# Kernel tuning notes

Hardware: AMD Instinct MI355X
Metric: run time of the kernel (lower is better)

Reference implementation:

```python
import jax, jax.numpy as jnp
import numpy as np

N = 8192
IN_F = 256
OUT_F = 128
ALPHA = 0.2
NEG = -9000000000000000.0

def setup_inputs() -> dict:
    key = jax.random.key(0)
    k1, k2, k3, k4 = jax.random.split(key, 4)
    h = jax.random.normal(k1, (N, IN_F), dtype=jnp.float32)
    adj = jax.random.randint(k2, (N, N), 0, 2, dtype=jnp.int32)
    # xavier-uniform-like params
    limW = float(np.sqrt(6.0 / (IN_F + OUT_F)))
    W = jax.random.uniform(k3, (IN_F, OUT_F), minval=-limW, maxval=limW, dtype=jnp.float32)
    lima = float(np.sqrt(6.0 / (2 * OUT_F + 1)))
    a = jax.random.uniform(k4, (2 * OUT_F, 1), minval=-lima, maxval=lima, dtype=jnp.float32)
    return {"h": h, "adj": adj, "W": W, "a": a}

def reference(h, adj, W, a):
    Wh = h @ W  # [N, F]
    # e_ij = LeakyReLU(a1.Wh_i + a2.Wh_j) -- avoids [N,N,2F] intermediate
    a1 = a[:OUT_F, 0]  # [F]
    a2 = a[OUT_F:, 0]  # [F]
    f1 = Wh @ a1  # [N]
    f2 = Wh @ a2  # [N]
    e = jax.nn.leaky_relu(f1[:, None] + f2[None, :], negative_slope=ALPHA)  # [N,N]
    att = jnp.where(adj > 0, e, jnp.float32(NEG))
    att = jax.nn.softmax(att, axis=1)
    h_prime = att @ Wh  # [N, F]
    return h_prime
```

## Files before the change

### kernel.cpp

```cpp
#include <hip/hip_runtime.h>
#include <hip/hip_bf16.h>

#define N    8192
#define INF  256
#define OUTF 128
#define ALPHA 0.2f
#define JS   8
#define NTS  (N / JS / 32)

typedef __attribute__((ext_vector_type(8))) short bf16x8;
typedef __attribute__((ext_vector_type(4))) float f32x4;

__device__ __forceinline__ unsigned short f2bf(float x) {
    union { float f; unsigned u; } v; v.f = x;
    unsigned r = v.u + 0x7fff + ((v.u >> 16) & 1);
    return (unsigned short)(r >> 16);
}

__device__ __forceinline__ void gll16(const void* g, void* l) {
    __builtin_amdgcn_global_load_lds(
        (const __attribute__((address_space(1))) unsigned*)g,
        (__attribute__((address_space(3))) unsigned*)l, 16, 0, 0);
}

__global__ __launch_bounds__(256) void k01_prep(
        const int* __restrict__ adj, unsigned* __restrict__ bits,
        const float* __restrict__ h, const float* __restrict__ W,
        const float* __restrict__ a,
        unsigned short* __restrict__ WhTb, float* __restrict__ f1, float* __restrict__ f2) {
    __shared__ float hs[8][INF];
    const int t = threadIdx.x;

    if (blockIdx.x >= 1024) {
        const size_t g = (size_t)(blockIdx.x - 1024) * 256 + t;
        const int4* p = (const int4*)adj + g * 8;
        unsigned b = 0;
        #pragma unroll
        for (int u = 0; u < 8; ++u) {
            int4 v = p[u];
            b |= (v.x > 0 ? 1u : 0u) << (u * 4 + 0);
            b |= (v.y > 0 ? 1u : 0u) << (u * 4 + 1);
            b |= (v.z > 0 ? 1u : 0u) << (u * 4 + 2);
            b |= (v.w > 0 ? 1u : 0u) << (u * 4 + 3);
        }
        bits[g] = b;
        return;
    }

    const int i0 = blockIdx.x * 8;
    #pragma unroll
    for (int u = 0; u < 2; ++u) {
        int idx = u * 256 + t;
        int r   = idx >> 6;
        int kq  = idx & 63;
        *(float4*)&hs[r][kq * 4] = *(const float4*)(h + (size_t)(i0 + r) * INF + kq * 4);
    }
    __syncthreads();

    const int rg = t >> 5;
    const int ct = t & 31;
    float acc[4] = {0.f, 0.f, 0.f, 0.f};

    #pragma unroll 8
    for (int k = 0; k < INF; ++k) {
        float4 wv = *(const float4*)(W + (size_t)k * OUTF + ct * 4);
        float  hx = hs[rg][k];
        acc[0] += hx * wv.x; acc[1] += hx * wv.y;
        acc[2] += hx * wv.z; acc[3] += hx * wv.w;
    }

    const int r0 = i0 + rg;
    const int jb = r0 >> 5;
    const int jo = r0 & 31;
    #pragma unroll
    for (int cc = 0; cc < 4; ++cc)
        WhTb[(size_t)jb * 4096 + (ct * 4 + cc) * 32 + jo] = f2bf(acc[cc]);

    const float4 a1v = *(const float4*)(a + ct * 4);
    const float4 a2v = *(const float4*)(a + OUTF + ct * 4);
    float p1 = acc[0]*a1v.x + acc[1]*a1v.y + acc[2]*a1v.z + acc[3]*a1v.w;
    float p2 = acc[0]*a2v.x + acc[1]*a2v.y + acc[2]*a2v.z + acc[3]*a2v.w;
    #pragma unroll
    for (int off = 16; off > 0; off >>= 1) {
        p1 += __shfl_down(p1, off, 32);
        p2 += __shfl_down(p2, off, 32);
    }
    if (ct == 0) { f1[r0] = p1; f2[r0] = p2; }
}

__device__ __forceinline__ float pbit(float f1r, float fv, unsigned byte_,
                                      int u, float& dsum) {
    float s = f1r + fv;
    float e = fmaxf(s, ALPHA * s);
    float p = (byte_ & (1u << u)) ? __expf(e) : 0.f;
    dsum += p;
    return p;
}

#define K2SUB(WORD, PH, JT)                                                  \
    {                                                                        \
        if ((JT) + 1 < NTS) {                                                \
            const char* ws_ = (const char*)WhTb + (size_t)(tile0 + (JT) + 1) * 8192; \
            char* bd_ = (char*)&bsm[(PH) ^ 1][0];                            \
            gll16(ws_ + t * 16,        bd_ + wv * 1024 + 0);                 \
            gll16(ws_ + 4096 + t * 16, bd_ + 4096 + wv * 1024 + 0);          \
        }                                                                    \
        float4 F0_ = *(const float4*)&f2s[(JT) * 32 + quad * 8];             \
        float4 F1_ = *(const float4*)&f2s[(JT) * 32 + quad * 8 + 4];         \
        unsigned byte_ = ((WORD) >> (quad << 3)) & 0xffu;                    \
        float p0_ = pbit(f1r, F0_.x, byte_, 0, dsum);                        \
        float p1_ = pbit(f1r, F0_.y, byte_, 1, dsum);                        \
        float p2_ = pbit(f1r, F0_.z, byte_, 2, dsum);                        \
        float p3_ = pbit(f1r, F0_.w, byte_, 3, dsum);                        \
        float p4_ = pbit(f1r, F1_.x, byte_, 4, dsum);                        \
        float p5_ = pbit(f1r, F1_.y, byte_, 5, dsum);                        \
        float p6_ = pbit(f1r, F1_.z, byte_, 6, dsum);                        \
        float p7_ = pbit(f1r, F1_.w, byte_, 7, dsum);                        \
        union { __hip_bfloat162 hh[4]; bf16x8 v; } pk_;                      \
        pk_.hh[0] = __float22bfloat162_rn(make_float2(p0_, p1_));            \
        pk_.hh[1] = __float22bfloat162_rn(make_float2(p2_, p3_));            \
        pk_.hh[2] = __float22bfloat162_rn(make_float2(p4_, p5_));            \
        pk_.hh[3] = __float22bfloat162_rn(make_float2(p6_, p7_));            \
        bf16x8 afrag = pk_.v;                                                \
        const char* bb_ = (const char*)&bsm[PH][0] + laneb2;                 \
        bf16x8 b0_ = *(const bf16x8*)(bb_);                                  \
        bf16x8 b1_ = *(const bf16x8*)(bb_ + 1024);                           \
        bf16x8 b2_ = *(const bf16x8*)(bb_ + 2048);                           \
        bf16x8 b3_ = *(const bf16x8*)(bb_ + 3072);                           \
        bf16x8 b4_ = *(const bf16x8*)(bb_ + 4096);                           \
        bf16x8 b5_ = *(const bf16x8*)(bb_ + 5120);                           \
        bf16x8 b6_ = *(const bf16x8*)(bb_ + 6144);                           \
        bf16x8 b7_ = *(const bf16x8*)(bb_ + 7168);                           \
        acc0 = __builtin_amdgcn_mfma_f32_16x16x32_bf16(afrag, b0_, acc0, 0, 0, 0); \
        acc1 = __builtin_amdgcn_mfma_f32_16x16x32_bf16(afrag, b1_, acc1, 0, 0, 0); \
        acc2 = __builtin_amdgcn_mfma_f32_16x16x32_bf16(afrag, b2_, acc2, 0, 0, 0); \
        acc3 = __builtin_amdgcn_mfma_f32_16x16x32_bf16(afrag, b3_, acc3, 0, 0, 0); \
        acc4 = __builtin_amdgcn_mfma_f32_16x16x32_bf16(afrag, b4_, acc4, 0, 0, 0); \
        acc5 = __builtin_amdgcn_mfma_f32_16x16x32_bf16(afrag, b5_, acc5, 0, 0, 0); \
        acc6 = __builtin_amdgcn_mfma_f32_16x16x32_bf16(afrag, b6_, acc6, 0, 0, 0); \
        acc7 = __builtin_amdgcn_mfma_f32_16x16x32_bf16(afrag, b7_, acc7, 0, 0, 0); \
        __syncthreads();                                                     \
    }

__global__ __launch_bounds__(256, 4) void k2_attn(
        const unsigned* __restrict__ bits, const unsigned short* __restrict__ WhTb,
        const float* __restrict__ f1, const float* __restrict__ f2,
        float* __restrict__ num, float* __restrict__ den) {
    __shared__ unsigned short bsm[2][4096];
    __shared__ float f2s[1024];

    const int t    = threadIdx.x;
    const int wv   = t >> 6;
    const int ln   = t & 63;
    const int m16  = ln & 15;
    const int quad = ln >> 4;
    const int i0   = blockIdx.x * 64;
    const int s    = blockIdx.y;
    const int row  = i0 + wv * 16 + m16;
    const int tile0 = s * NTS;
    const int j0    = s * (N / JS);
    const int laneb2 = (m16 * 32 + quad * 8) * 2;

    *(float4*)&f2s[t * 4] = *(const float4*)(f2 + j0 + t * 4);
    {
        const char* ws0 = (const char*)WhTb + (size_t)tile0 * 8192;
        char* bd = (char*)&bsm[0][0];
        gll16(ws0 + t * 16,        bd + wv * 1024);
        gll16(ws0 + 4096 + t * 16, bd + 4096 + wv * 1024);
    }

    const float f1r = f1[row];
    const uint4* brow = (const uint4*)(bits + (size_t)row * 256 + tile0);

    f32x4 acc0 = {0.f,0.f,0.f,0.f}, acc1 = {0.f,0.f,0.f,0.f};
    f32x4 acc2 = {0.f,0.f,0.f,0.f}, acc3 = {0.f,0.f,0.f,0.f};
    f32x4 acc4 = {0.f,0.f,0.f,0.f}, acc5 = {0.f,0.f,0.f,0.f};
    f32x4 acc6 = {0.f,0.f,0.f,0.f}, acc7 = {0.f,0.f,0.f,0.f};
    float dsum = 0.f;

    uint4 bwc = brow[0];
    __syncthreads();

    for (int g = 0; g < NTS / 4; ++g) {
        uint4 bwn = brow[(g + 1 < NTS / 4) ? g + 1 : g];
        const int jtb = g * 4;
        K2SUB(bwc.x, 0, jtb + 0)
        K2SUB(bwc.y, 1, jtb + 1)
        K2SUB(bwc.z, 0, jtb + 2)
        K2SUB(bwc.w, 1, jtb + 3)
        bwc = bwn;
    }

    dsum += __shfl_xor(dsum, 16);
    dsum += __shfl_xor(dsum, 32);
    if (quad == 0) den[(size_t)s * N + row] = dsum;

    float* np = num + (size_t)s * N * OUTF;
    #pragma unroll
    for (int r = 0; r < 4; ++r) {
        const size_t orow = (size_t)(i0 + wv * 16 + quad * 4 + r) * OUTF;
        np[orow + 0 * 16 + m16] = acc0[r];
        np[orow + 1 * 16 + m16] = acc1[r];
        np[orow + 2 * 16 + m16] = acc2[r];
        np[orow + 3 * 16 + m16] = acc3[r];
        np[orow + 4 * 16 + m16] = acc4[r];
        np[orow + 5 * 16 + m16] = acc5[r];
        np[orow + 6 * 16 + m16] = acc6[r];
        np[orow + 7 * 16 + m16] = acc7[r];
    }
}

__global__ __launch_bounds__(256) void k3_combine(
        const float* __restrict__ num, const float* __restrict__ den,
        float* __restrict__ out) {
    const int idx = blockIdx.x * 256 + threadIdx.x;
    const int row = idx >> 5;
    const int c4  = (idx & 31) * 4;
    float4 ns = {0.f,0.f,0.f,0.f};
    float  ds = 0.f;
    #pragma unroll
    for (int s = 0; s < JS; ++s) {
        float4 nv = *(const float4*)(num + ((size_t)s * N + row) * OUTF + c4);
        ns.x += nv.x; ns.y += nv.y; ns.z += nv.z; ns.w += nv.w;
        ds += den[(size_t)s * N + row];
    }
    const float inv = 1.0f / ds;
    float4 o = {ns.x * inv, ns.y * inv, ns.z * inv, ns.w * inv};
    *(float4*)(out + (size_t)row * OUTF + c4) = o;
}

extern "C" void kernel_launch(void* const* d_in, const int* in_sizes, int n_in,
                              void* d_out, int out_size, void* d_ws, size_t ws_size,
                              hipStream_t stream) {
    const float* h   = (const float*)d_in[0];
    const int*   adj = (const int*)  d_in[1];
    const float* W   = (const float*)d_in[2];
    const float* a   = (const float*)d_in[3];
    float* out = (float*)d_out;

    unsigned short* WhTb = (unsigned short*)d_ws;
    float*    f1   = (float*)(WhTb + (size_t)N * OUTF);
    float*    f2   = f1 + N;
    float*    den  = f2 + N;
    unsigned* bits = (unsigned*)(den + (size_t)JS * N);
    float*    num  = (float*)(bits + (size_t)N * (N / 32));

    k01_prep  <<<1024 + (N / 32) * (N / 256), 256, 0, stream>>>(adj, bits, h, W, a, WhTb, f1, f2);
    k2_attn   <<<dim3(N / 64, JS), 256, 0, stream>>>(bits, WhTb, f1, f2, num, den);
    k3_combine<<<(N * OUTF / 4) / 256, 256, 0, stream>>>(num, den, out);
}
```

Measured before the change: 431.4 us.

## Quad-buffer Wh tiles with prefetch distance two, vmcnt waits, and swizzled LDS layout

Grows the LDS staging of Wh tiles from two to four buffers and prefetches two tiles ahead instead of one. The per-step __syncthreads is replaced with explicit s_waitcnt vmcnt plus s_barrier, so each step waits only for the tile it is about to use. It also XOR-swizzles the global source offsets and LDS read addresses to cut bank conflicts on the bf16x8 fragment loads. The loop is peeled so the last steps drain with smaller vmcnt values. This relies on hand-counted outstanding-load numbers, uses more LDS, and drops the barrier that previously guarded buffer reuse.

Measured after the change: 430.4 us. No clear change (-0.2%).

```diff
diff --git a/kernel.cpp b/kernel.cpp
--- a/kernel.cpp
+++ b/kernel.cpp
@@ -97,13 +97,17 @@
     return p;
 }
 
-#define K2SUB(WORD, PH, JT)                                                  \
+#define VMB4 "s_waitcnt vmcnt(4)\n\ts_barrier"
+#define VMB2 "s_waitcnt vmcnt(2)\n\ts_barrier"
+#define VMB0 "s_waitcnt vmcnt(0)\n\ts_barrier"
+
+#define K2STEP(WORD, O, JT, VMB, ISSUE)                                      \
     {                                                                        \
-        if ((JT) + 1 < NTS) {                                                \
-            const char* ws_ = (const char*)WhTb + (size_t)(tile0 + (JT) + 1) * 8192; \
-            char* bd_ = (char*)&bsm[(PH) ^ 1][0];                            \
-            gll16(ws_ + t * 16,        bd_ + wv * 1024 + 0);                 \
-            gll16(ws_ + 4096 + t * 16, bd_ + 4096 + wv * 1024 + 0);          \
+        if (ISSUE) {                                                         \
+            const char* ws_ = (const char*)WhTb + (size_t)(tile0 + (JT) + 2) * 8192; \
+            char* bd_ = (char*)&bsm[((O) + 2) & 3][0];                       \
+            gll16(ws_ + tsw,        bd_ + wv * 1024);                        \
+            gll16(ws_ + 4096 + tsw, bd_ + 4096 + wv * 1024);                 \
         }                                                                    \
         float4 F0_ = *(const float4*)&f2s[(JT) * 32 + quad * 8];             \
         float4 F1_ = *(const float4*)&f2s[(JT) * 32 + quad * 8 + 4];         \
@@ -122,7 +126,8 @@
         pk_.hh[2] = __float22bfloat162_rn(make_float2(p4_, p5_));            \
         pk_.hh[3] = __float22bfloat162_rn(make_float2(p6_, p7_));            \
         bf16x8 afrag = pk_.v;                                                \
-        const char* bb_ = (const char*)&bsm[PH][0] + laneb2;                 \
+        asm volatile(VMB ::: "memory");                                      \
+        const char* bb_ = (const char*)&bsm[(O)][0] + laneb2;                \
         bf16x8 b0_ = *(const bf16x8*)(bb_);                                  \
         bf16x8 b1_ = *(const bf16x8*)(bb_ + 1024);                           \
         bf16x8 b2_ = *(const bf16x8*)(bb_ + 2048);                           \
@@ -139,14 +144,13 @@
         acc5 = __builtin_amdgcn_mfma_f32_16x16x32_bf16(afrag, b5_, acc5, 0, 0, 0); \
         acc6 = __builtin_amdgcn_mfma_f32_16x16x32_bf16(afrag, b6_, acc6, 0, 0, 0); \
         acc7 = __builtin_amdgcn_mfma_f32_16x16x32_bf16(afrag, b7_, acc7, 0, 0, 0); \
-        __syncthreads();                                                     \
     }
 
 __global__ __launch_bounds__(256, 4) void k2_attn(
         const unsigned* __restrict__ bits, const unsigned short* __restrict__ WhTb,
         const float* __restrict__ f1, const float* __restrict__ f2,
         float* __restrict__ num, float* __restrict__ den) {
-    __shared__ unsigned short bsm[2][4096];
+    __shared__ unsigned short bsm[4][4096];
     __shared__ float f2s[1024];
 
     const int t    = threadIdx.x;
@@ -159,14 +163,19 @@
     const int row  = i0 + wv * 16 + m16;
     const int tile0 = s * NTS;
     const int j0    = s * (N / JS);
-    const int laneb2 = (m16 * 32 + quad * 8) * 2;
+    const int laneb2 = m16 * 64 + ((quad ^ ((m16 >> 1) & 3)) << 4);
+    const int tsw = (t * 16) ^ (((t >> 3) & 3) << 4);
 
     *(float4*)&f2s[t * 4] = *(const float4*)(f2 + j0 + t * 4);
     {
         const char* ws0 = (const char*)WhTb + (size_t)tile0 * 8192;
-        char* bd = (char*)&bsm[0][0];
-        gll16(ws0 + t * 16,        bd + wv * 1024);
-        gll16(ws0 + 4096 + t * 16, bd + 4096 + wv * 1024);
+        char* bd0 = (char*)&bsm[0][0];
+        gll16(ws0 + tsw,        bd0 + wv * 1024);
+        gll16(ws0 + 4096 + tsw, bd0 + 4096 + wv * 1024);
+        const char* ws1 = ws0 + 8192;
+        char* bd1 = (char*)&bsm[1][0];
+        gll16(ws1 + tsw,        bd1 + wv * 1024);
+        gll16(ws1 + 4096 + tsw, bd1 + 4096 + wv * 1024);
     }
 
     const float f1r = f1[row];
@@ -179,17 +188,21 @@
     float dsum = 0.f;
 
     uint4 bwc = brow[0];
-    __syncthreads();
-
-    for (int g = 0; g < NTS / 4; ++g) {
-        uint4 bwn = brow[(g + 1 < NTS / 4) ? g + 1 : g];
+    asm volatile("s_waitcnt lgkmcnt(0)\n\ts_barrier" ::: "memory");
+
+    for (int g = 0; g < 7; ++g) {
+        uint4 bwn = brow[g + 1];
         const int jtb = g * 4;
-        K2SUB(bwc.x, 0, jtb + 0)
-        K2SUB(bwc.y, 1, jtb + 1)
-        K2SUB(bwc.z, 0, jtb + 2)
-        K2SUB(bwc.w, 1, jtb + 3)
+        K2STEP(bwc.x, 0, jtb + 0, VMB4, 1)
+        K2STEP(bwc.y, 1, jtb + 1, VMB4, 1)
+        K2STEP(bwc.z, 2, jtb + 2, VMB4, 1)
+        K2STEP(bwc.w, 3, jtb + 3, VMB4, 1)
         bwc = bwn;
     }
+    K2STEP(bwc.x, 0, 28, VMB4, 1)
+    K2STEP(bwc.y, 1, 29, VMB4, 1)
+    K2STEP(bwc.z, 2, 30, VMB2, 0)
+    K2STEP(bwc.w, 3, 31, VMB0, 0)
 
     dsum += __shfl_xor(dsum, 16);
     dsum += __shfl_xor(dsum, 32);
```

## Load Wh B-fragments directly from global memory, dropping LDS staging and barriers

Applied to the files above, without the earlier changes.

Each wave now reads its MFMA B operand fragments straight from global (L2-cached) memory instead of staging the Wh tile into double-buffered LDS via global_load_lds. This removes the per-subtile __syncthreads and the LDS round trip, letting the four waves run independently. In exchange, every wave issues its own redundant global loads of the same tile, and load latency is no longer hidden by an explicit prefetch stage.

Measured after the change: 467.7 us. 8.4% more time.

```diff
diff --git a/kernel.cpp b/kernel.cpp
--- a/kernel.cpp
+++ b/kernel.cpp
@@ -15,12 +15,6 @@
     union { float f; unsigned u; } v; v.f = x;
     unsigned r = v.u + 0x7fff + ((v.u >> 16) & 1);
     return (unsigned short)(r >> 16);
-}
-
-__device__ __forceinline__ void gll16(const void* g, void* l) {
-    __builtin_amdgcn_global_load_lds(
-        (const __attribute__((address_space(1))) unsigned*)g,
-        (__attribute__((address_space(3))) unsigned*)l, 16, 0, 0);
 }
 
 __global__ __launch_bounds__(256) void k01_prep(
@@ -97,14 +91,17 @@
     return p;
 }
 
-#define K2SUB(WORD, PH, JT)                                                  \
+#define K2L(WORD, JT)                                                        \
     {                                                                        \
-        if ((JT) + 1 < NTS) {                                                \
-            const char* ws_ = (const char*)WhTb + (size_t)(tile0 + (JT) + 1) * 8192; \
-            char* bd_ = (char*)&bsm[(PH) ^ 1][0];                            \
-            gll16(ws_ + t * 16,        bd_ + wv * 1024 + 0);                 \
-            gll16(ws_ + 4096 + t * 16, bd_ + 4096 + wv * 1024 + 0);          \
-        }                                                                    \
+        const bf16x8* bp_ = (const bf16x8*)(WhTb + (size_t)(tile0 + (JT)) * 4096) + boff; \
+        bf16x8 b0_ = bp_[0 * 64];                                            \
+        bf16x8 b1_ = bp_[1 * 64];                                            \
+        bf16x8 b2_ = bp_[2 * 64];                                            \
+        bf16x8 b3_ = bp_[3 * 64];                                            \
+        bf16x8 b4_ = bp_[4 * 64];                                            \
+        bf16x8 b5_ = bp_[5 * 64];                                            \
+        bf16x8 b6_ = bp_[6 * 64];                                            \
+        bf16x8 b7_ = bp_[7 * 64];                                            \
         float4 F0_ = *(const float4*)&f2s[(JT) * 32 + quad * 8];             \
         float4 F1_ = *(const float4*)&f2s[(JT) * 32 + quad * 8 + 4];         \
         unsigned byte_ = ((WORD) >> (quad << 3)) & 0xffu;                    \
@@ -122,15 +119,6 @@
         pk_.hh[2] = __float22bfloat162_rn(make_float2(p4_, p5_));            \
         pk_.hh[3] = __float22bfloat162_rn(make_float2(p6_, p7_));            \
         bf16x8 afrag = pk_.v;                                                \
-        const char* bb_ = (const char*)&bsm[PH][0] + laneb2;                 \
-        bf16x8 b0_ = *(const bf16x8*)(bb_);                                  \
-        bf16x8 b1_ = *(const bf16x8*)(bb_ + 1024);                           \
-        bf16x8 b2_ = *(const bf16x8*)(bb_ + 2048);                           \
-        bf16x8 b3_ = *(const bf16x8*)(bb_ + 3072);                           \
-        bf16x8 b4_ = *(const bf16x8*)(bb_ + 4096);                           \
-        bf16x8 b5_ = *(const bf16x8*)(bb_ + 5120);                           \
-        bf16x8 b6_ = *(const bf16x8*)(bb_ + 6144);                           \
-        bf16x8 b7_ = *(const bf16x8*)(bb_ + 7168);                           \
         acc0 = __builtin_amdgcn_mfma_f32_16x16x32_bf16(afrag, b0_, acc0, 0, 0, 0); \
         acc1 = __builtin_amdgcn_mfma_f32_16x16x32_bf16(afrag, b1_, acc1, 0, 0, 0); \
         acc2 = __builtin_amdgcn_mfma_f32_16x16x32_bf16(afrag, b2_, acc2, 0, 0, 0); \
@@ -139,14 +127,12 @@
         acc5 = __builtin_amdgcn_mfma_f32_16x16x32_bf16(afrag, b5_, acc5, 0, 0, 0); \
         acc6 = __builtin_amdgcn_mfma_f32_16x16x32_bf16(afrag, b6_, acc6, 0, 0, 0); \
         acc7 = __builtin_amdgcn_mfma_f32_16x16x32_bf16(afrag, b7_, acc7, 0, 0, 0); \
-        __syncthreads();                                                     \
     }
 
 __global__ __launch_bounds__(256, 4) void k2_attn(
         const unsigned* __restrict__ bits, const unsigned short* __restrict__ WhTb,
         const float* __restrict__ f1, const float* __restrict__ f2,
         float* __restrict__ num, float* __restrict__ den) {
-    __shared__ unsigned short bsm[2][4096];
     __shared__ float f2s[1024];
 
     const int t    = threadIdx.x;
@@ -159,15 +145,9 @@
     const int row  = i0 + wv * 16 + m16;
     const int tile0 = s * NTS;
     const int j0    = s * (N / JS);
-    const int laneb2 = (m16 * 32 + quad * 8) * 2;
+    const int boff = m16 * 4 + quad;
 
     *(float4*)&f2s[t * 4] = *(const float4*)(f2 + j0 + t * 4);
-    {
-        const char* ws0 = (const char*)WhTb + (size_t)tile0 * 8192;
-        char* bd = (char*)&bsm[0][0];
-        gll16(ws0 + t * 16,        bd + wv * 1024);
-        gll16(ws0 + 4096 + t * 16, bd + 4096 + wv * 1024);
-    }
 
     const float f1r = f1[row];
     const uint4* brow = (const uint4*)(bits + (size_t)row * 256 + tile0);
@@ -184,10 +164,10 @@
     for (int g = 0; g < NTS / 4; ++g) {
         uint4 bwn = brow[(g + 1 < NTS / 4) ? g + 1 : g];
         const int jtb = g * 4;
-        K2SUB(bwc.x, 0, jtb + 0)
-        K2SUB(bwc.y, 1, jtb + 1)
-        K2SUB(bwc.z, 0, jtb + 2)
-        K2SUB(bwc.w, 1, jtb + 3)
+        K2L(bwc.x, jtb + 0)
+        K2L(bwc.y, jtb + 1)
+        K2L(bwc.z, jtb + 2)
+        K2L(bwc.w, jtb + 3)
         bwc = bwn;
     }
 
```

## Double LDS tile size, swizzle layout, and halve barriers in attention loop

Applied to the files above, without the earlier changes.

The attention kernel now stages two 32-column Wh tiles per LDS buffer, so each barrier covers two MFMA sub-steps instead of one, halving the number of __syncthreads. The LDS tile is XOR-swizzled on both the global_load_lds side and the MFMA read side to avoid bank conflicts. The generic __syncthreads is replaced with explicit s_waitcnt vmcnt(0) plus s_barrier. In exchange it doubles LDS use per block, which may limit occupancy, and it relies on hand-placed waitcnt correctness.

New measurement: 435.0 us. No clear change (+0.8%).

```diff
diff --git a/kernel.cpp b/kernel.cpp
--- a/kernel.cpp
+++ b/kernel.cpp
@@ -97,16 +97,10 @@
     return p;
 }
 
-#define K2SUB(WORD, PH, JT)                                                  \
+#define KSUB(WORD, KS, JT)                                                   \
     {                                                                        \
-        if ((JT) + 1 < NTS) {                                                \
-            const char* ws_ = (const char*)WhTb + (size_t)(tile0 + (JT) + 1) * 8192; \
-            char* bd_ = (char*)&bsm[(PH) ^ 1][0];                            \
-            gll16(ws_ + t * 16,        bd_ + wv * 1024 + 0);                 \
-            gll16(ws_ + 4096 + t * 16, bd_ + 4096 + wv * 1024 + 0);          \
-        }                                                                    \
-        float4 F0_ = *(const float4*)&f2s[(JT) * 32 + quad * 8];             \
-        float4 F1_ = *(const float4*)&f2s[(JT) * 32 + quad * 8 + 4];         \
+        float4 F0_ = *(const float4*)&f2s[((JT) * 2 + (KS)) * 32 + quad * 8]; \
+        float4 F1_ = *(const float4*)&f2s[((JT) * 2 + (KS)) * 32 + quad * 8 + 4]; \
         unsigned byte_ = ((WORD) >> (quad << 3)) & 0xffu;                    \
         float p0_ = pbit(f1r, F0_.x, byte_, 0, dsum);                        \
         float p1_ = pbit(f1r, F0_.y, byte_, 1, dsum);                        \
@@ -122,7 +116,7 @@
         pk_.hh[2] = __float22bfloat162_rn(make_float2(p4_, p5_));            \
         pk_.hh[3] = __float22bfloat162_rn(make_float2(p6_, p7_));            \
         bf16x8 afrag = pk_.v;                                                \
-        const char* bb_ = (const char*)&bsm[PH][0] + laneb2;                 \
+        const char* bb_ = bbase + (KS) * 8192 + laneb2;                      \
         bf16x8 b0_ = *(const bf16x8*)(bb_);                                  \
         bf16x8 b1_ = *(const bf16x8*)(bb_ + 1024);                           \
         bf16x8 b2_ = *(const bf16x8*)(bb_ + 2048);                           \
@@ -139,14 +133,28 @@
         acc5 = __builtin_amdgcn_mfma_f32_16x16x32_bf16(afrag, b5_, acc5, 0, 0, 0); \
         acc6 = __builtin_amdgcn_mfma_f32_16x16x32_bf16(afrag, b6_, acc6, 0, 0, 0); \
         acc7 = __builtin_amdgcn_mfma_f32_16x16x32_bf16(afrag, b7_, acc7, 0, 0, 0); \
-        __syncthreads();                                                     \
+    }
+
+#define K2STEP(W0, W1, O, JT, ISSG)                                          \
+    {                                                                        \
+        asm volatile("s_waitcnt vmcnt(0)\n\ts_barrier" ::: "memory");        \
+        if (ISSG) {                                                          \
+            const char* ws_ = (const char*)WhTb                              \
+                + (size_t)(tile0 + ((JT) + 1) * 2) * 8192 + wv * 4096 + lsw; \
+            char* bd_ = (char*)&bsm[(O) ^ 1][0] + wv * 4096;                 \
+            gll16(ws_,        bd_);        gll16(ws_ + 1024, bd_ + 1024);    \
+            gll16(ws_ + 2048, bd_ + 2048); gll16(ws_ + 3072, bd_ + 3072);    \
+        }                                                                    \
+        const char* bbase = (const char*)&bsm[(O)][0];                       \
+        KSUB(W0, 0, JT)                                                      \
+        KSUB(W1, 1, JT)                                                      \
     }
 
 __global__ __launch_bounds__(256, 4) void k2_attn(
         const unsigned* __restrict__ bits, const unsigned short* __restrict__ WhTb,
         const float* __restrict__ f1, const float* __restrict__ f2,
         float* __restrict__ num, float* __restrict__ den) {
-    __shared__ unsigned short bsm[2][4096];
+    __shared__ unsigned short bsm[2][8192];
     __shared__ float f2s[1024];
 
     const int t    = threadIdx.x;
@@ -159,14 +167,15 @@
     const int row  = i0 + wv * 16 + m16;
     const int tile0 = s * NTS;
     const int j0    = s * (N / JS);
-    const int laneb2 = (m16 * 32 + quad * 8) * 2;
+    const int laneb2 = m16 * 64 + ((quad ^ ((m16 >> 1) & 3)) << 4);
+    const int lsw = (ln * 16) ^ (((ln >> 3) & 3) << 4);
 
     *(float4*)&f2s[t * 4] = *(const float4*)(f2 + j0 + t * 4);
     {
-        const char* ws0 = (const char*)WhTb + (size_t)tile0 * 8192;
-        char* bd = (char*)&bsm[0][0];
-        gll16(ws0 + t * 16,        bd + wv * 1024);
-        gll16(ws0 + 4096 + t * 16, bd + 4096 + wv * 1024);
+        const char* ws0 = (const char*)WhTb + (size_t)tile0 * 8192 + wv * 4096 + lsw;
+        char* bd0 = (char*)&bsm[0][0] + wv * 4096;
+        gll16(ws0,        bd0);        gll16(ws0 + 1024, bd0 + 1024);
+        gll16(ws0 + 2048, bd0 + 2048); gll16(ws0 + 3072, bd0 + 3072);
     }
 
     const float f1r = f1[row];
@@ -179,15 +188,13 @@
     float dsum = 0.f;
 
     uint4 bwc = brow[0];
-    __syncthreads();
-
-    for (int g = 0; g < NTS / 4; ++g) {
-        uint4 bwn = brow[(g + 1 < NTS / 4) ? g + 1 : g];
-        const int jtb = g * 4;
-        K2SUB(bwc.x, 0, jtb + 0)
-        K2SUB(bwc.y, 1, jtb + 1)
-        K2SUB(bwc.z, 0, jtb + 2)
-        K2SUB(bwc.w, 1, jtb + 3)
+    asm volatile("s_waitcnt lgkmcnt(0)\n\ts_barrier" ::: "memory");
+
+    for (int g = 0; g < 8; ++g) {
+        const int jt = g * 2;
+        K2STEP(bwc.x, bwc.y, 0, jt, 1)
+        uint4 bwn = brow[(g + 1 < 8) ? g + 1 : g];
+        K2STEP(bwc.z, bwc.w, 1, jt + 1, (g < 7))
         bwc = bwn;
     }
 
```
